# Performance work log

Hardware: AMD Instinct MI355X
Metric: run time of the kernel (lower is better)

The kernel has to match this reference:

```python
import jax, jax.numpy as jnp
import numpy as np

IGNORE_IDX = -100
DELTA_V = 0.5
DELTA_D = 1.5
PARAM_VAR = 1.0
PARAM_DIST = 1.0
PARAM_REG = 0.001
LOSS_WEIGHT = 1.0
K = 64  # static upper bound on number of instances (matches fill_max of instance_labels)


def setup_inputs() -> dict:
    key = jax.random.key(0)
    k1, k2, k3 = jax.random.split(key, 3)
    B, D, N = 8, 32, 131072
    embedding_logits = jax.random.normal(k1, (B, D, N), dtype=jnp.float32)
    semantic_labels = jax.random.randint(k2, (B, N), 0, 21, dtype=jnp.int64)
    instance_labels = jax.random.randint(k3, (B, N), 0, K, dtype=jnp.int64)
    return {
        "embedding_logits": embedding_logits,
        "semantic_labels": semantic_labels,
        "instance_labels": instance_labels,
        "feature_dim": D,
    }


def _single(x, cls, inst):
    # x: [N, D] embeddings, cls/inst: [N] int labels
    dtype = x.dtype
    valid = cls != IGNORE_IDX
    # points of class 1 are merged into instance 0 (intent of the torch code)
    inst = jnp.where(cls == 1, 0, inst)
    ids = jnp.where(valid, inst, K)  # invalid points -> extra bin K

    counts = jax.ops.segment_sum(valid.astype(dtype), ids, num_segments=K + 1)[:K]
    seg_sum = jax.ops.segment_sum(
        jnp.where(valid[:, None], x, jnp.zeros((), dtype)), ids, num_segments=K + 1
    )[:K]                                            # [K, D]
    mu = seg_sum / (counts[:, None] + 1e-8)          # [K, D] cluster means
    present = counts > 0                             # [K]
    n_inst = jnp.maximum(jnp.sum(present.astype(dtype)), 1.0)

    # intra-cluster variance term (L1 distance to own cluster mean, hinged)
    mu_pt = mu[jnp.clip(ids, 0, K - 1)]              # [N, D]
    d = jnp.sum(jnp.abs(x - mu_pt), axis=1)          # [N]
    d = jnp.square(jnp.maximum(d - DELTA_V, 0.0)) * valid.astype(dtype)
    l_var_seg = jax.ops.segment_sum(d, ids, num_segments=K + 1)[:K] / (counts + 1e-8)
    l_var = jnp.sum(l_var_seg) / n_inst

    # inter-cluster distance term over distinct present cluster pairs
    pdist = jnp.sum(jnp.abs(mu[:, None, :] - mu[None, :, :]), axis=-1)  # [K, K]
    pair_mask = present[:, None] & present[None, :] & ~jnp.eye(K, dtype=bool)
    hinge = jnp.square(jnp.maximum(2.0 * DELTA_D - pdist, 0.0)) * pair_mask.astype(dtype)
    npairs = jnp.sum(pair_mask.astype(dtype))
    l_dist = jnp.where(npairs > 0, jnp.sum(hinge) / jnp.maximum(npairs, 1.0), 0.0)

    # regularization: mean L1 norm of present cluster means
    l_reg = jnp.sum(jnp.sum(jnp.abs(mu), axis=1) * present.astype(dtype)) / n_inst

    l_var = PARAM_VAR * l_var
    l_dist = PARAM_DIST * l_dist
    l_reg = PARAM_REG * l_reg
    loss = LOSS_WEIGHT * (l_var + l_dist + l_reg)
    return loss, l_var, l_dist, l_reg


def reference(embedding_logits, semantic_labels, instance_labels, feature_dim):
    # embedding_logits: [B, D, N] -> per-point embeddings [B, N, D]
    x = jnp.transpose(embedding_logits, (0, 2, 1))
    loss, l_var, l_dist, l_reg = jax.vmap(_single)(x, semantic_labels, instance_labels)
    return (
        jnp.mean(loss),
        jnp.mean(l_var),
        jnp.mean(l_dist),
        jnp.mean(l_reg),
    )
```

## Files before the change

### kernel.cpp

```cpp
#include <hip/hip_runtime.h>


typedef unsigned char uchar;
typedef __attribute__((ext_vector_type(8)))  short bf16x8;
typedef __attribute__((ext_vector_type(16))) float f32x16;

#define IGNORE_IDX (-100)

constexpr int B = 8;
constexpr int D = 32;
constexpr int K = 64;
constexpr int NPTS = 131072;
constexpr int BPB  = 128;
constexpr int SPAN = 1024;
constexpr float DELTA_V = 0.5f;
constexpr float TWO_DELTA_D = 3.0f;
constexpr float PARAM_REG = 0.001f;

constexpr size_t OFF_CNT = (size_t)B * 2048;
constexpr size_t OFF_VS  = OFF_CNT + (size_t)B * K;
constexpr size_t OFF_ID  = OFF_VS  + (size_t)B * K;
constexpr size_t ZERO_FLOATS = OFF_ID;

__device__ inline unsigned bfpack(unsigned a0, unsigned a1) {
    return __builtin_amdgcn_perm(a1, a0, 0x07060302u);
}

__global__ __launch_bounds__(256) void k1_fused(
    const float* __restrict__ x, const int* __restrict__ sem,
    const int* __restrict__ inst, uchar* __restrict__ id8,
    int* __restrict__ cnt, float* __restrict__ musum)
{
    __shared__ __align__(16) char s_mem[32768];
    __shared__ unsigned s_id4[256];
    __shared__ int s_cnt[K];
    const int t = threadIdx.x, w = t >> 6, L = t & 63;
    const int g = L >> 5, ln = L & 31;
    const unsigned lnu = (unsigned)ln, lnp32 = (unsigned)(ln + 32);
    const int blk = blockIdx.x, b = blk >> 7, sp = blk & (BPB - 1);

    if (t < K) s_cnt[t] = 0;
    __syncthreads();

    {
        const size_t off = (size_t)b * NPTS + sp * SPAN + t * 4;
        const int4 c4 = *(const int4*)(sem + off);
        const int4 i4 = *(const int4*)(inst + off);
        const int cl[4] = {c4.x, c4.y, c4.z, c4.w};
        const int il[4] = {i4.x, i4.y, i4.z, i4.w};
        unsigned wrd = 0;
#pragma unroll
        for (int j = 0; j < 4; ++j) {
            const bool v = (cl[j] != IGNORE_IDX);
            int q = (cl[j] == 1) ? 0 : il[j];
            q = (q < 0) ? 0 : (q > K - 1 ? K - 1 : q);
            if (v) atomicAdd(&s_cnt[q], 1);
            wrd |= (v ? (unsigned)q : 255u) << (8 * j);
        }
        s_id4[t] = wrd;
        *(unsigned*)(id8 + off) = wrd;
    }

    f32x16 acc0, acc1;
#pragma unroll
    for (int i = 0; i < 16; ++i) { acc0[i] = 0.f; acc1[i] = 0.f; }

    const unsigned* xb = (const unsigned*)(x + (size_t)b * D * NPTS + sp * SPAN);

    uint4 pf[8];
#pragma unroll
    for (int P = 0; P < 8; ++P)
        pf[P] = *(const uint4*)(xb + (size_t)(P * 4 + w) * NPTS + L * 4);

    for (int st = 0; st < 4; ++st) {
#pragma unroll
        for (int P = 0; P < 8; ++P) {
            const int row = P * 4 + w;
            const unsigned u0 = bfpack(pf[P].x + 0x8000u, pf[P].y + 0x8000u);
            const unsigned u1 = bfpack(pf[P].z + 0x8000u, pf[P].w + 0x8000u);
            const int waddr = row * 512 + (((L >> 1) ^ (row & 7)) * 16) + (L & 1) * 8;
            *(uint2*)(s_mem + waddr) = make_uint2(u0, u1);
        }
        if (st < 3) {
#pragma unroll
            for (int P = 0; P < 8; ++P)
                pf[P] = *(const uint4*)(xb + (size_t)(P * 4 + w) * NPTS
                                        + (st + 1) * 256 + L * 4);
        }
        __syncthreads();

#pragma unroll
        for (int cc = 0; cc < 4; ++cc) {
            const int K16 = (w * 4 + cc) * 2 + g;
            const int raddr = ln * 512 + ((K16 ^ (ln & 7)) * 16);
            const bf16x8 Af = *(const bf16x8*)(s_mem + raddr);

            const int n0 = st * 256 + (w * 4 + cc) * 16 + g * 8;
            const uint2 idq = *(const uint2*)(&s_id4[n0 >> 2]);
            union { unsigned u[4]; bf16x8 v; } B0, B1;
#pragma unroll
            for (int p = 0; p < 4; ++p) {
                const unsigned pair = ((p < 2) ? idq.x : idq.y) >> ((p & 1) * 16);
                const unsigned e0 = pair & 255u, e1 = (pair >> 8) & 255u;
                unsigned r0 = (e0 == lnu)   ? 0x3F80u : 0u;
                unsigned r1 = (e0 == lnp32) ? 0x3F80u : 0u;
                if (e1 == lnu)   r0 |= 0x3F800000u;
                if (e1 == lnp32) r1 |= 0x3F800000u;
                B0.u[p] = r0; B1.u[p] = r1;
            }
            acc0 = __builtin_amdgcn_mfma_f32_32x32x16_bf16(Af, B0.v, acc0, 0, 0, 0);
            acc1 = __builtin_amdgcn_mfma_f32_32x32x16_bf16(Af, B1.v, acc1, 0, 0, 0);
        }
        __syncthreads();
    }

    float (*s_part)[2048] = (float(*)[2048])s_mem;
#pragma unroll
    for (int r = 0; r < 16; ++r) {
        const int row = (r & 3) + 8 * (r >> 2) + 4 * g;
        s_part[w][row * 64 + ln]      = acc0[r];
        s_part[w][row * 64 + ln + 32] = acc1[r];
    }
    __syncthreads();

    float* dst = musum + (size_t)b * 2048;
    for (int i = t; i < 2048; i += 256)
        unsafeAtomicAdd(&dst[i],
            s_part[0][i] + s_part[1][i] + s_part[2][i] + s_part[3][i]);
    if (t < K) {
        const int c = s_cnt[t];
        if (c) atomicAdd(&cnt[b * K + t], c);
    }
}

__global__ __launch_bounds__(256) void k3_var(
    const float* __restrict__ x, const uchar* __restrict__ id8,
    const float* __restrict__ musum, const int* __restrict__ cnt,
    float* __restrict__ vsum)
{
    __shared__ float s_mu[2048];
    __shared__ float s_var[K];
    const int t = threadIdx.x;
    const int blk = blockIdx.x, b = blk >> 7, sp = blk & (BPB - 1);

    if (t < K) s_var[t] = 0.f;
    for (int i = t; i < 2048; i += 256)
        s_mu[i] = musum[(size_t)b * 2048 + i]
                / ((float)cnt[b * K + (i & 63)] + 1e-8f);

    const unsigned idw = *(const unsigned*)(id8 + (size_t)b * NPTS + sp * SPAN + t * 4);
    int q[4]; bool val[4];
#pragma unroll
    for (int j = 0; j < 4; ++j) {
        const unsigned e = (idw >> (8 * j)) & 255u;
        val[j] = (e < 64u);
        q[j] = (int)(e & 63u);
    }
    __syncthreads();

    const float* xp = x + (size_t)b * D * NPTS + sp * SPAN + t * 4;
    float s0 = 0.f, s1 = 0.f, s2 = 0.f, s3 = 0.f;
#pragma unroll
    for (int d = 0; d < D; ++d) {
        const float4 xv = *(const float4*)(xp + (size_t)d * NPTS);
        s0 += fabsf(xv.x - s_mu[d * 64 + q[0]]);
        s1 += fabsf(xv.y - s_mu[d * 64 + q[1]]);
        s2 += fabsf(xv.z - s_mu[d * 64 + q[2]]);
        s3 += fabsf(xv.w - s_mu[d * 64 + q[3]]);
    }

    const float ss[4] = {s0, s1, s2, s3};
#pragma unroll
    for (int j = 0; j < 4; ++j) {
        if (val[j]) {
            const float h = fmaxf(ss[j] - DELTA_V, 0.f);
            if (h > 0.f) unsafeAtomicAdd(&s_var[q[j]], h * h);
        }
    }
    __syncthreads();
    if (t < K) {
        const float v = s_var[t];
        if (v != 0.f) unsafeAtomicAdd(&vsum[b * K + t], v);
    }
}

__device__ float block_reduce_sum512(float v, float* s_buf) {
    for (int o = 32; o > 0; o >>= 1) v += __shfl_down(v, o, 64);
    const int wid  = threadIdx.x >> 6;
    const int lane = threadIdx.x & 63;
    if (lane == 0) s_buf[wid] = v;
    __syncthreads();
    float r = 0.f;
    if (threadIdx.x == 0)
        for (int w = 0; w < 8; ++w) r += s_buf[w];
    __syncthreads();
    return r;
}

__global__ __launch_bounds__(512) void k4_final(const float* __restrict__ musum,
                                                const int* __restrict__ cnt,
                                                const float* __restrict__ vsum,
                                                float* __restrict__ out)
{
    const int b = blockIdx.x;
    __shared__ float s_mu[K][D + 1];
    __shared__ float s_cnt[K];
    __shared__ float s_red[8];

    const int t = threadIdx.x;
    if (t < K) s_cnt[t] = (float)cnt[b * K + t];
    for (int i = t; i < K * D; i += 512) {
        const int d = i >> 6, k = i & 63;
        s_mu[k][d] = musum[(size_t)b * 2048 + i]
                   / ((float)cnt[b * K + k] + 1e-8f);
    }
    __syncthreads();

    float distPart = 0.f;
    for (int p = t; p < K * K; p += 512) {
        const int i = p >> 6, j = p & 63;
        if (i != j && s_cnt[i] > 0.f && s_cnt[j] > 0.f) {
            float dsum = 0.f;
#pragma unroll
            for (int d = 0; d < D; ++d) dsum += fabsf(s_mu[i][d] - s_mu[j][d]);
            const float h = fmaxf(TWO_DELTA_D - dsum, 0.f);
            distPart += h * h;
        }
    }
    float regPart = 0.f;
    for (int i = t; i < K * D; i += 512) {
        const int k = i >> 5;
        if (s_cnt[k] > 0.f) regPart += fabsf(s_mu[k][i & 31]);
    }
    float varPart = 0.f, npPart = 0.f;
    if (t < K) {
        varPart = vsum[b * K + t] / (s_cnt[t] + 1e-8f);
        npPart  = (s_cnt[t] > 0.f) ? 1.f : 0.f;
    }

    const float distSum = block_reduce_sum512(distPart, s_red);
    const float regSum  = block_reduce_sum512(regPart,  s_red);
    const float varSum  = block_reduce_sum512(varPart,  s_red);
    const float npSum   = block_reduce_sum512(npPart,   s_red);

    if (t == 0) {
        const float n_inst = fmaxf(npSum, 1.0f);
        const float npairs = npSum * npSum - npSum;
        const float l_var  = varSum / n_inst;
        const float l_dist = (npairs > 0.f) ? (distSum / fmaxf(npairs, 1.0f)) : 0.f;
        const float l_reg  = PARAM_REG * (regSum / n_inst);
        const float invB   = 1.0f / (float)B;
        unsafeAtomicAdd(out + 0, (l_var + l_dist + l_reg) * invB);
        unsafeAtomicAdd(out + 1, l_var  * invB);
        unsafeAtomicAdd(out + 2, l_dist * invB);
        unsafeAtomicAdd(out + 3, l_reg  * invB);
    }
}

extern "C" void kernel_launch(void* const* d_in, const int* in_sizes, int n_in,
                              void* d_out, int out_size, void* d_ws, size_t ws_size,
                              hipStream_t stream) {
    const float* x    = (const float*)d_in[0];
    const int*   sem  = (const int*)d_in[1];
    const int*   inst = (const int*)d_in[2];
    float*       out  = (float*)d_out;
    float*       ws   = (float*)d_ws;

    float* musum = ws;
    int*   cnt   = (int*)(ws + OFF_CNT);
    float* vsum  = ws + OFF_VS;
    uchar* id8   = (uchar*)(ws + OFF_ID);

    hipMemsetAsync(ws, 0, ZERO_FLOATS * sizeof(float), stream);
    hipMemsetAsync(out, 0, (size_t)out_size * sizeof(float), stream);

    k1_fused<<<dim3(B * BPB), dim3(256), 0, stream>>>(x, sem, inst, id8, cnt, musum);
    k3_var  <<<dim3(B * BPB), dim3(256), 0, stream>>>(x, id8, musum, cnt, vsum);
    k4_final<<<dim3(B), dim3(512), 0, stream>>>(musum, cnt, vsum, out);
}
```

Baseline: 248.1 us.

## Replace memsets with id-prep kernel and fuse final reduction via last-block ticket

Adds a k0_ids kernel that zeroes the workspace and output and builds the packed 8-bit instance ids, replacing two hipMemsetAsync calls. k1 now reads the precomputed ids instead of the label arrays. The separate final kernel is folded into k3_var through an atomic ticket, so the last block per batch computes the loss terms. This cuts launch and memset overhead, but adds a kernel boundary before k1 and serialises the final work into one block per batch.

```diff
diff --git a/kernel.cpp b/kernel.cpp
--- a/kernel.cpp
+++ b/kernel.cpp
@@ -19,16 +19,46 @@
 
 constexpr size_t OFF_CNT = (size_t)B * 2048;
 constexpr size_t OFF_VS  = OFF_CNT + (size_t)B * K;
-constexpr size_t OFF_ID  = OFF_VS  + (size_t)B * K;
-constexpr size_t ZERO_FLOATS = OFF_ID;
+constexpr size_t OFF_TK  = OFF_VS  + (size_t)B * K;
+constexpr size_t OFF_ID  = OFF_TK + 8;
+constexpr int ZERO_FLOATS = 17416;
 
 __device__ inline unsigned bfpack(unsigned a0, unsigned a1) {
     return __builtin_amdgcn_perm(a1, a0, 0x07060302u);
 }
 
+__global__ __launch_bounds__(256) void k0_ids(
+    const int* __restrict__ sem, const int* __restrict__ inst,
+    uchar* __restrict__ id8, float* __restrict__ zbuf, float* __restrict__ out)
+{
+    const int t = threadIdx.x, blk = blockIdx.x;
+    const int zi = blk * 256 + t;
+    if (zi < ZERO_FLOATS) zbuf[zi] = 0.f;
+    if (blk == 100 && t < 4) out[t] = 0.f;
+
+    const int base = blk * 2048 + t * 8;
+    const int4 c0 = *(const int4*)(sem + base);
+    const int4 c1 = *(const int4*)(sem + base + 4);
+    const int4 i0 = *(const int4*)(inst + base);
+    const int4 i1 = *(const int4*)(inst + base + 4);
+    const int cl[8] = {c0.x, c0.y, c0.z, c0.w, c1.x, c1.y, c1.z, c1.w};
+    const int il[8] = {i0.x, i0.y, i0.z, i0.w, i1.x, i1.y, i1.z, i1.w};
+
+    unsigned w0 = 0, w1 = 0;
+#pragma unroll
+    for (int j = 0; j < 8; ++j) {
+        const bool v = (cl[j] != IGNORE_IDX);
+        int q = (cl[j] == 1) ? 0 : il[j];
+        q = (q < 0) ? 0 : (q > K - 1 ? K - 1 : q);
+        const unsigned byte = v ? (unsigned)q : 255u;
+        if (j < 4) w0 |= byte << (8 * j);
+        else       w1 |= byte << (8 * (j - 4));
+    }
+    *(uint2*)(id8 + base) = make_uint2(w0, w1);
+}
+
 __global__ __launch_bounds__(256) void k1_fused(
-    const float* __restrict__ x, const int* __restrict__ sem,
-    const int* __restrict__ inst, uchar* __restrict__ id8,
+    const float* __restrict__ x, const uchar* __restrict__ id8,
     int* __restrict__ cnt, float* __restrict__ musum)
 {
     __shared__ __align__(16) char s_mem[32768];
@@ -44,21 +74,13 @@
 
     {
         const size_t off = (size_t)b * NPTS + sp * SPAN + t * 4;
-        const int4 c4 = *(const int4*)(sem + off);
-        const int4 i4 = *(const int4*)(inst + off);
-        const int cl[4] = {c4.x, c4.y, c4.z, c4.w};
-        const int il[4] = {i4.x, i4.y, i4.z, i4.w};
-        unsigned wrd = 0;
+        const unsigned wrd = *(const unsigned*)(id8 + off);
+        s_id4[t] = wrd;
 #pragma unroll
         for (int j = 0; j < 4; ++j) {
-            const bool v = (cl[j] != IGNORE_IDX);
-            int q = (cl[j] == 1) ? 0 : il[j];
-            q = (q < 0) ? 0 : (q > K - 1 ? K - 1 : q);
-            if (v) atomicAdd(&s_cnt[q], 1);
-            wrd |= (v ? (unsigned)q : 255u) << (8 * j);
-        }
-        s_id4[t] = wrd;
-        *(unsigned*)(id8 + off) = wrd;
+            const unsigned e = (wrd >> (8 * j)) & 255u;
+            if (e < 64u) atomicAdd(&s_cnt[e], 1);
+        }
     }
 
     f32x16 acc0, acc1;
@@ -133,13 +155,31 @@
     }
 }
 
+__device__ float block_reduce_sum256(float v, float* s_buf) {
+    for (int o = 32; o > 0; o >>= 1) v += __shfl_down(v, o, 64);
+    const int wid  = threadIdx.x >> 6;
+    const int lane = threadIdx.x & 63;
+    if (lane == 0) s_buf[wid] = v;
+    __syncthreads();
+    float r = 0.f;
+    if (threadIdx.x == 0)
+        for (int w = 0; w < 4; ++w) r += s_buf[w];
+    __syncthreads();
+    return r;
+}
+
 __global__ __launch_bounds__(256) void k3_var(
     const float* __restrict__ x, const uchar* __restrict__ id8,
     const float* __restrict__ musum, const int* __restrict__ cnt,
-    float* __restrict__ vsum)
+    float* __restrict__ vsum, int* __restrict__ ticket, float* __restrict__ out)
 {
-    __shared__ float s_mu[2048];
-    __shared__ float s_var[K];
+    __shared__ float s_pool[2112];
+    __shared__ float s_fc[K];
+    __shared__ float s_red[4];
+    __shared__ int   s_last;
+    float* s_mu  = s_pool;
+    float* s_var = s_pool + 2048;
+
     const int t = threadIdx.x;
     const int blk = blockIdx.x, b = blk >> 7, sp = blk & (BPB - 1);
 
@@ -182,66 +222,50 @@
         const float v = s_var[t];
         if (v != 0.f) unsafeAtomicAdd(&vsum[b * K + t], v);
     }
-}
-
-__device__ float block_reduce_sum512(float v, float* s_buf) {
-    for (int o = 32; o > 0; o >>= 1) v += __shfl_down(v, o, 64);
-    const int wid  = threadIdx.x >> 6;
-    const int lane = threadIdx.x & 63;
-    if (lane == 0) s_buf[wid] = v;
-    __syncthreads();
-    float r = 0.f;
-    if (threadIdx.x == 0)
-        for (int w = 0; w < 8; ++w) r += s_buf[w];
-    __syncthreads();
-    return r;
-}
-
-__global__ __launch_bounds__(512) void k4_final(const float* __restrict__ musum,
-                                                const int* __restrict__ cnt,
-                                                const float* __restrict__ vsum,
-                                                float* __restrict__ out)
-{
-    const int b = blockIdx.x;
-    __shared__ float s_mu[K][D + 1];
-    __shared__ float s_cnt[K];
-    __shared__ float s_red[8];
-
-    const int t = threadIdx.x;
-    if (t < K) s_cnt[t] = (float)cnt[b * K + t];
-    for (int i = t; i < K * D; i += 512) {
+
+    __threadfence();
+    __syncthreads();
+    if (t == 0) s_last = (atomicAdd(&ticket[b], 1) == BPB - 1) ? 1 : 0;
+    __syncthreads();
+    if (!s_last) return;
+    __threadfence();
+
+    if (t < K) s_fc[t] = (float)cnt[b * K + t];
+    __syncthreads();
+    for (int i = t; i < 2048; i += 256) {
         const int d = i >> 6, k = i & 63;
-        s_mu[k][d] = musum[(size_t)b * 2048 + i]
-                   / ((float)cnt[b * K + k] + 1e-8f);
+        s_pool[k * 33 + d] = musum[(size_t)b * 2048 + i]
+                           / ((float)cnt[b * K + k] + 1e-8f);
     }
     __syncthreads();
 
     float distPart = 0.f;
-    for (int p = t; p < K * K; p += 512) {
+    for (int p = t; p < K * K; p += 256) {
         const int i = p >> 6, j = p & 63;
-        if (i != j && s_cnt[i] > 0.f && s_cnt[j] > 0.f) {
+        if (i != j && s_fc[i] > 0.f && s_fc[j] > 0.f) {
             float dsum = 0.f;
 #pragma unroll
-            for (int d = 0; d < D; ++d) dsum += fabsf(s_mu[i][d] - s_mu[j][d]);
+            for (int d = 0; d < D; ++d)
+                dsum += fabsf(s_pool[i * 33 + d] - s_pool[j * 33 + d]);
             const float h = fmaxf(TWO_DELTA_D - dsum, 0.f);
             distPart += h * h;
         }
     }
     float regPart = 0.f;
-    for (int i = t; i < K * D; i += 512) {
+    for (int i = t; i < K * D; i += 256) {
         const int k = i >> 5;
-        if (s_cnt[k] > 0.f) regPart += fabsf(s_mu[k][i & 31]);
+        if (s_fc[k] > 0.f) regPart += fabsf(s_pool[k * 33 + (i & 31)]);
     }
     float varPart = 0.f, npPart = 0.f;
     if (t < K) {
-        varPart = vsum[b * K + t] / (s_cnt[t] + 1e-8f);
-        npPart  = (s_cnt[t] > 0.f) ? 1.f : 0.f;
-    }
-
-    const float distSum = block_reduce_sum512(distPart, s_red);
-    const float regSum  = block_reduce_sum512(regPart,  s_red);
-    const float varSum  = block_reduce_sum512(varPart,  s_red);
-    const float npSum   = block_reduce_sum512(npPart,   s_red);
+        varPart = vsum[b * K + t] / (s_fc[t] + 1e-8f);
+        npPart  = (s_fc[t] > 0.f) ? 1.f : 0.f;
+    }
+
+    const float distSum = block_reduce_sum256(distPart, s_red);
+    const float regSum  = block_reduce_sum256(regPart,  s_red);
+    const float varSum  = block_reduce_sum256(varPart,  s_red);
+    const float npSum   = block_reduce_sum256(npPart,   s_red);
 
     if (t == 0) {
         const float n_inst = fmaxf(npSum, 1.0f);
@@ -266,15 +290,13 @@
     float*       out  = (float*)d_out;
     float*       ws   = (float*)d_ws;
 
-    float* musum = ws;
-    int*   cnt   = (int*)(ws + OFF_CNT);
-    float* vsum  = ws + OFF_VS;
-    uchar* id8   = (uchar*)(ws + OFF_ID);
-
-    hipMemsetAsync(ws, 0, ZERO_FLOATS * sizeof(float), stream);
-    hipMemsetAsync(out, 0, (size_t)out_size * sizeof(float), stream);
-
-    k1_fused<<<dim3(B * BPB), dim3(256), 0, stream>>>(x, sem, inst, id8, cnt, musum);
-    k3_var  <<<dim3(B * BPB), dim3(256), 0, stream>>>(x, id8, musum, cnt, vsum);
-    k4_final<<<dim3(B), dim3(512), 0, stream>>>(musum, cnt, vsum, out);
-}
+    float* musum  = ws;
+    int*   cnt    = (int*)(ws + OFF_CNT);
+    float* vsum   = ws + OFF_VS;
+    int*   ticket = (int*)(ws + OFF_TK);
+    uchar* id8    = (uchar*)(ws + OFF_ID);
+
+    k0_ids  <<<dim3(B * NPTS / 2048), dim3(256), 0, stream>>>(sem, inst, id8, ws, out);
+    k1_fused<<<dim3(B * BPB), dim3(256), 0, stream>>>(x, id8, cnt, musum);
+    k3_var  <<<dim3(B * BPB), dim3(256), 0, stream>>>(x, id8, musum, cnt, vsum, ticket, out);
+}
```

New measurement: 358.5 us. +44.5%, slower.
